# Kernel optimization log

Hardware: AMD Instinct MI355X
Metric: run time of the kernel (lower is better)

## Reference

```python
import jax, jax.numpy as jnp
import numpy as np

B, N, D = 64, 576, 768   # batch, num_patches (24x24), embed_dim
K = 1024                 # n_pairs
NUM_TARGETS = 2


def setup_inputs() -> dict:
    key = jax.random.key(0)
    k1, k2, k3, k4 = jax.random.split(key, 4)
    z = jax.random.normal(k1, (B, N, D), dtype=jnp.float32)
    indices = jax.random.randint(k2, (B, K, 2), 0, N, dtype=jnp.int64)
    # head params: nn.Linear(2*embed_dim, num_targets)
    W = jax.random.normal(k3, (2 * D, NUM_TARGETS), dtype=jnp.float32) * 0.02
    b_head = jax.random.normal(k4, (NUM_TARGETS,), dtype=jnp.float32) * 0.02
    return {"z": z, "indices": indices, "W": W, "b_head": b_head}


def reference(z, indices, W, b_head):
    b, n, d = z.shape
    k = indices.shape[1]
    # index_pairs: gather both patches of each pair -> [b, k, 2, d]
    batch_idx = jnp.arange(b)[:, None, None]            # [b,1,1]
    z_pairs = z[batch_idx, indices]                     # [b, k, 2, d]
    # pairwise_mlp head: concat pair along feature dim, tiny linear
    out = z_pairs.reshape(b, k, 2 * d) @ W + b_head     # [b, k, num_targets]
    return out, indices
```

## Files before the change

### kernel.cpp

```cpp
#include <hip/hip_runtime.h>

#define BB 64
#define NN 576
#define DD 768
#define KK 1024
#define ROWS (BB * NN)
#define PAIRS (BB * KK)

__global__ __launch_bounds__(1024) void partvit_fused(const float* __restrict__ z,
                                                      const int* __restrict__ idx,
                                                      const float* __restrict__ W,
                                                      const float* __restrict__ bh,
                                                      float* __restrict__ out) {
    __shared__ float4 P[NN];
    const int b    = blockIdx.x;
    const int lane = threadIdx.x & 63;
    const int wave = threadIdx.x >> 6;

    const float2* __restrict__ W2 = (const float2*)W;
    float2 wa[3][4], wb[3][4];
#pragma unroll
    for (int j = 0; j < 3; ++j) {
#pragma unroll
        for (int c = 0; c < 4; ++c) {
            const int d = j * 256 + (lane << 2) + c;
            wa[j][c] = W2[d];
            wb[j][c] = W2[d + DD];
        }
    }

    const float4* __restrict__ z4 = (const float4*)z + (size_t)b * NN * 192;

    for (int r = wave; r < NN; r += 32) {
        const int r2 = r + 16;
        float4 v0[3], v1[3];
#pragma unroll
        for (int j = 0; j < 3; ++j) v0[j] = z4[r  * 192 + j * 64 + lane];
#pragma unroll
        for (int j = 0; j < 3; ++j) v1[j] = z4[r2 * 192 + j * 64 + lane];

        float a00 = 0.f, a01 = 0.f, a10 = 0.f, a11 = 0.f;
        float c00 = 0.f, c01 = 0.f, c10 = 0.f, c11 = 0.f;
#pragma unroll
        for (int j = 0; j < 3; ++j) {
            a00 = fmaf(v0[j].x, wa[j][0].x, a00);
            a00 = fmaf(v0[j].y, wa[j][1].x, a00);
            a00 = fmaf(v0[j].z, wa[j][2].x, a00);
            a00 = fmaf(v0[j].w, wa[j][3].x, a00);
            a01 = fmaf(v0[j].x, wa[j][0].y, a01);
            a01 = fmaf(v0[j].y, wa[j][1].y, a01);
            a01 = fmaf(v0[j].z, wa[j][2].y, a01);
            a01 = fmaf(v0[j].w, wa[j][3].y, a01);
            a10 = fmaf(v0[j].x, wb[j][0].x, a10);
            a10 = fmaf(v0[j].y, wb[j][1].x, a10);
            a10 = fmaf(v0[j].z, wb[j][2].x, a10);
            a10 = fmaf(v0[j].w, wb[j][3].x, a10);
            a11 = fmaf(v0[j].x, wb[j][0].y, a11);
            a11 = fmaf(v0[j].y, wb[j][1].y, a11);
            a11 = fmaf(v0[j].z, wb[j][2].y, a11);
            a11 = fmaf(v0[j].w, wb[j][3].y, a11);

            c00 = fmaf(v1[j].x, wa[j][0].x, c00);
            c00 = fmaf(v1[j].y, wa[j][1].x, c00);
            c00 = fmaf(v1[j].z, wa[j][2].x, c00);
            c00 = fmaf(v1[j].w, wa[j][3].x, c00);
            c01 = fmaf(v1[j].x, wa[j][0].y, c01);
            c01 = fmaf(v1[j].y, wa[j][1].y, c01);
            c01 = fmaf(v1[j].z, wa[j][2].y, c01);
            c01 = fmaf(v1[j].w, wa[j][3].y, c01);
            c10 = fmaf(v1[j].x, wb[j][0].x, c10);
            c10 = fmaf(v1[j].y, wb[j][1].x, c10);
            c10 = fmaf(v1[j].z, wb[j][2].x, c10);
            c10 = fmaf(v1[j].w, wb[j][3].x, c10);
            c11 = fmaf(v1[j].x, wb[j][0].y, c11);
            c11 = fmaf(v1[j].y, wb[j][1].y, c11);
            c11 = fmaf(v1[j].z, wb[j][2].y, c11);
            c11 = fmaf(v1[j].w, wb[j][3].y, c11);
        }
#pragma unroll
        for (int off = 32; off > 0; off >>= 1) {
            a00 += __shfl_xor(a00, off, 64);
            a01 += __shfl_xor(a01, off, 64);
            a10 += __shfl_xor(a10, off, 64);
            a11 += __shfl_xor(a11, off, 64);
            c00 += __shfl_xor(c00, off, 64);
            c01 += __shfl_xor(c01, off, 64);
            c10 += __shfl_xor(c10, off, 64);
            c11 += __shfl_xor(c11, off, 64);
        }
        if (lane == 0) {
            P[r]  = make_float4(a00, a01, a10, a11);
            P[r2] = make_float4(c00, c01, c10, c11);
        }
    }

    __syncthreads();

    const int t = b * KK + (int)threadIdx.x;
    const int2 id = ((const int2*)idx)[t];
    const int i0 = min(max(id.x, 0), NN - 1);
    const int i1 = min(max(id.y, 0), NN - 1);
    const float4 p0 = P[i0];
    const float4 p1 = P[i1];
    const float b0 = bh[0], b1 = bh[1];
    ((float2*)out)[t] = make_float2(p0.x + p1.z + b0, p0.y + p1.w + b1);
    ((float2*)out)[PAIRS + t] = make_float2((float)id.x, (float)id.y);
}

extern "C" void kernel_launch(void* const* d_in, const int* in_sizes, int n_in,
                              void* d_out, int out_size, void* d_ws, size_t ws_size,
                              hipStream_t stream) {
    const float* z   = (const float*)d_in[0];
    const int*   idx = (const int*)d_in[1];
    const float* W   = (const float*)d_in[2];
    const float* bh  = (const float*)d_in[3];
    float*       out = (float*)d_out;
    (void)d_ws; (void)ws_size; (void)in_sizes; (void)n_in; (void)out_size;

    partvit_fused<<<BB, 1024, 0, stream>>>(z, idx, W, bh, out);
}
```

Measured before the change: 188.0 us.

## Spread projection over 256 blocks with global grid barrier before pair gather

Projects all patch rows across 256 blocks of 512 threads instead of 64 blocks, writing per-row partial products to a global buffer. A global atomic-counter barrier with spin-wait then separates this phase from the pair-gather phase. The aim is to fill more of the GPU's compute units for the memory-bound z read. In exchange it relies on all 256 blocks being co-resident, and the barrier has a spin timeout that could let blocks proceed before the data is ready.

```diff
diff --git a/kernel.cpp b/kernel.cpp
--- a/kernel.cpp
+++ b/kernel.cpp
@@ -7,13 +7,21 @@
 #define ROWS (BB * NN)
 #define PAIRS (BB * KK)
 
-__global__ __launch_bounds__(1024) void partvit_fused(const float* __restrict__ z,
-                                                      const int* __restrict__ idx,
-                                                      const float* __restrict__ W,
-                                                      const float* __restrict__ bh,
-                                                      float* __restrict__ out) {
-    __shared__ float4 P[NN];
-    const int b    = blockIdx.x;
+#define NBLK 256
+#define TPB  512
+#define ROWS_PER_BLK (ROWS / NBLK)
+#define ROWS_PER_WAVE (ROWS_PER_BLK / (TPB/64))
+#define PAIRS_PER_BLK (PAIRS / NBLK)
+
+__device__ float4   g_P[ROWS];
+__device__ unsigned g_ctr = 0;
+
+__global__ __launch_bounds__(TPB)
+void partvit_onekernel(const float* __restrict__ z,
+                       const int* __restrict__ idx,
+                       const float* __restrict__ W,
+                       const float* __restrict__ bh,
+                       float* __restrict__ out) {
     const int lane = threadIdx.x & 63;
     const int wave = threadIdx.x >> 6;
 
@@ -29,10 +37,13 @@
         }
     }
 
-    const float4* __restrict__ z4 = (const float4*)z + (size_t)b * NN * 192;
+    const float4* __restrict__ z4 = (const float4*)z;
+    const int rbase = blockIdx.x * ROWS_PER_BLK + wave * ROWS_PER_WAVE;
 
-    for (int r = wave; r < NN; r += 32) {
-        const int r2 = r + 16;
+#pragma unroll 1
+    for (int i = 0; i < ROWS_PER_WAVE; i += 2) {
+        const int r  = rbase + i;
+        const int r2 = r + 1;
         float4 v0[3], v1[3];
 #pragma unroll
         for (int j = 0; j < 3; ++j) v0[j] = z4[r  * 192 + j * 64 + lane];
@@ -89,22 +100,38 @@
             c11 += __shfl_xor(c11, off, 64);
         }
         if (lane == 0) {
-            P[r]  = make_float4(a00, a01, a10, a11);
-            P[r2] = make_float4(c00, c01, c10, c11);
+            g_P[r]  = make_float4(a00, a01, a10, a11);
+            g_P[r2] = make_float4(c00, c01, c10, c11);
         }
     }
 
     __syncthreads();
+    if (threadIdx.x == 0) {
+        __threadfence();
+        const unsigned old = atomicAdd(&g_ctr, 1u);
+        const unsigned target = (old & ~255u) + 256u;
+        int spins = 0;
+        while (__hip_atomic_load(&g_ctr, __ATOMIC_RELAXED,
+                                 __HIP_MEMORY_SCOPE_AGENT) < target) {
+            if (++spins > (1 << 18)) break;
+            __builtin_amdgcn_s_sleep(2);
+        }
+        __threadfence();
+    }
+    __syncthreads();
 
-    const int t = b * KK + (int)threadIdx.x;
-    const int2 id = ((const int2*)idx)[t];
-    const int i0 = min(max(id.x, 0), NN - 1);
-    const int i1 = min(max(id.y, 0), NN - 1);
-    const float4 p0 = P[i0];
-    const float4 p1 = P[i1];
-    const float b0 = bh[0], b1 = bh[1];
-    ((float2*)out)[t] = make_float2(p0.x + p1.z + b0, p0.y + p1.w + b1);
-    ((float2*)out)[PAIRS + t] = make_float2((float)id.x, (float)id.y);
+    if (threadIdx.x < PAIRS_PER_BLK) {
+        const int t = blockIdx.x * PAIRS_PER_BLK + (int)threadIdx.x;
+        const int2 id = ((const int2*)idx)[t];
+        const int i0 = min(max(id.x, 0), NN - 1);
+        const int i1 = min(max(id.y, 0), NN - 1);
+        const int b = t >> 10;
+        const float4 p0 = g_P[b * NN + i0];
+        const float4 p1 = g_P[b * NN + i1];
+        const float b0 = bh[0], b1 = bh[1];
+        ((float2*)out)[t] = make_float2(p0.x + p1.z + b0, p0.y + p1.w + b1);
+        ((float2*)out)[PAIRS + t] = make_float2((float)id.x, (float)id.y);
+    }
 }
 
 extern "C" void kernel_launch(void* const* d_in, const int* in_sizes, int n_in,
@@ -117,5 +144,5 @@
     float*       out = (float*)d_out;
     (void)d_ws; (void)ws_size; (void)in_sizes; (void)n_in; (void)out_size;
 
-    partvit_fused<<<BB, 1024, 0, stream>>>(z, idx, W, bh, out);
+    partvit_onekernel<<<NBLK, TPB, 0, stream>>>(z, idx, W, bh, out);
 }
```

Result: no change. 190.8 us (+1.5%).
